# Kernel optimization log

Hardware: AMD Instinct MI355X
Metric: run time of the kernel (lower is better)

Reference implementation:

```python
import jax, jax.numpy as jnp
import numpy as np

H = 1024      # hidden_size
NH = 16       # num_attention_heads
DK = H // NH  # head dim
C = 1024      # cyclic_size


def setup_inputs() -> dict:
    key = jax.random.key(0)
    ks = jax.random.split(key, 13)
    B, S = 2, 2048
    s = 1.0 / np.sqrt(H)
    inp = {
        "q": jax.random.normal(ks[0], (B, S, H), jnp.float32),
        "k": jax.random.normal(ks[1], (B, S, H), jnp.float32),
        "v": jax.random.normal(ks[2], (B, S, H), jnp.float32),
        "Wq": jax.random.normal(ks[3], (H, H), jnp.float32) * s,
        "bq": jnp.zeros((H,), jnp.float32),
        "Wk": jax.random.normal(ks[4], (H, H), jnp.float32) * s,
        "bk": jnp.zeros((H,), jnp.float32),
        "Wv": jax.random.normal(ks[5], (H, H), jnp.float32) * s,
        "bv": jnp.zeros((H,), jnp.float32),
        "Wo": jax.random.normal(ks[6], (H, H), jnp.float32) * s,
        "bo": jnp.zeros((H,), jnp.float32),
        "Wc": jax.random.normal(ks[7], (H, C), jnp.float32) * s,
        "bc": jnp.zeros((C,), jnp.float32),
    }
    return inp


def _split_heads(x):
    B, S, _ = x.shape
    return x.reshape(B, S, NH, DK).transpose(0, 2, 1, 3)  # [B,NH,S,DK]


def reference(q, k, v, Wq, bq, Wk, bk, Wv, bv, Wo, bo, Wc, bc):
    Q = _split_heads(q @ Wq + bq)
    K = _split_heads(k @ Wk + bk)
    V = _split_heads(v @ Wv + bv)
    # unfused SDPA: full [B,NH,S,S] scores, as in the original module
    scores = jnp.einsum("bhqd,bhkd->bhqk", Q, K) / jnp.sqrt(jnp.float32(DK))
    probs = jax.nn.softmax(scores, axis=-1)
    attn = jnp.einsum("bhqk,bhkd->bhqd", probs, V)  # [B,NH,S,DK]
    B, _, S, _ = attn.shape
    merged = attn.transpose(0, 2, 1, 3).reshape(B, S, H)
    h = merged @ Wo + bo
    c = merged @ Wc + bc
    return (c, h)
```

## Files before the change

kernel.cpp:

```cpp
#include <hip/hip_runtime.h>
#include <stdint.h>

typedef unsigned short u16;
typedef short bf16x8 __attribute__((ext_vector_type(8)));
typedef short bf16x4 __attribute__((ext_vector_type(4)));
typedef float f32x4 __attribute__((ext_vector_type(4)));

#define MB (1u<<20)
#define CL2 0.18033688f

static __device__ __forceinline__ u16 f2bf(float x){
  union { float f; unsigned u; } v; v.f = x;
  return (u16)((v.u + 0x7FFFu + ((v.u >> 16) & 1u)) >> 16);
}

static __device__ __forceinline__ void gld_lds16(const void* g, void* l){
  __builtin_amdgcn_global_load_lds((const __attribute__((address_space(1))) unsigned int*)g,
                                   (__attribute__((address_space(3))) unsigned int*)l, 16, 0, 0);
}

__global__ void convx(const float* __restrict__ q, const float* __restrict__ k, const float* __restrict__ v,
                      u16* __restrict__ qb, u16* __restrict__ kb, u16* __restrict__ vb){
  const float* s = blockIdx.z==0 ? q : (blockIdx.z==1 ? k : v);
  u16* d = blockIdx.z==0 ? qb : (blockIdx.z==1 ? kb : vb);
  int i = (blockIdx.x*256 + threadIdx.x)*4;
  float4 f = *(const float4*)(s + i);
  ushort4 o; o.x=f2bf(f.x); o.y=f2bf(f.y); o.z=f2bf(f.z); o.w=f2bf(f.w);
  *(ushort4*)(d + i) = o;
}

__global__ void convw(const float* W0,const float* W1,const float* W2,const float* W3,const float* W4,
                      u16* T0,u16* T1,u16* T2,u16* T3,u16* T4){
  const float* W = blockIdx.z==0?W0:blockIdx.z==1?W1:blockIdx.z==2?W2:blockIdx.z==3?W3:W4;
  u16* T = blockIdx.z==0?T0:blockIdx.z==1?T1:blockIdx.z==2?T2:blockIdx.z==3?T3:T4;
  __shared__ u16 t[64][65];
  int k0 = blockIdx.x*64, n0 = blockIdx.y*64;
  for (int i=0;i<16;i++){
    int idx = i*256 + threadIdx.x;
    int r = idx >> 6, c = idx & 63;
    t[r][c] = f2bf(W[(size_t)(k0+r)*1024 + n0 + c]);
  }
  __syncthreads();
  for (int i=0;i<2;i++){
    int idx = i*256 + threadIdx.x;
    int nl = idx >> 3, kc = idx & 7;
    bf16x8 o;
    #pragma unroll
    for (int j=0;j<8;j++) o[j] = (short)t[kc*8+j][nl];
    *(bf16x8*)(T + (size_t)(n0+nl)*1024 + k0 + kc*8) = o;
  }
}

template<int MODE>
static __device__ __forceinline__ void gemm_bt_dev(const u16* __restrict__ A, const u16* __restrict__ Bt,
                                                   const float* __restrict__ bias, void* __restrict__ Cout){
  __shared__ u16 As[128*32];
  __shared__ u16 Bs[128*32];
  const int tid = threadIdx.x, lane = tid & 63, w = tid >> 6;
  const int wm = w >> 1, wn = w & 1, quad = lane >> 4, lr = lane & 15;
  const int m0 = blockIdx.y * 128, n0 = blockIdx.x * 128;
  f32x4 acc[4][4] = {};
  const u16* Ab = A + (size_t)m0*1024;
  const u16* Bb = Bt + (size_t)n0*1024;
  const int srow = w*16 + (lane>>2);
  const int sg   = (lane & 3);
  for (int k0 = 0; k0 < 1024; k0 += 32){
    #pragma unroll
    for (int r = 0; r < 2; ++r){
      int row = r*64 + srow;
      int g = sg ^ ((row>>1)&3);
      gld_lds16(Ab + (size_t)row*1024 + k0 + g*8, As + (r*64 + w*16)*32);
      gld_lds16(Bb + (size_t)row*1024 + k0 + g*8, Bs + (r*64 + w*16)*32);
    }
    __syncthreads();
    bf16x8 af[4], bfr[4];
    #pragma unroll
    for (int i=0;i<4;i++){
      int rowa = wm*64 + i*16 + lr;
      af[i] = *(const bf16x8*)(As + rowa*32 + ((quad ^ ((rowa>>1)&3))*8));
      int rowb = wn*64 + i*16 + lr;
      bfr[i] = *(const bf16x8*)(Bs + rowb*32 + ((quad ^ ((rowb>>1)&3))*8));
    }
    #pragma unroll
    for (int mi=0;mi<4;mi++)
      #pragma unroll
      for (int ni=0;ni<4;ni++)
        acc[mi][ni] = __builtin_amdgcn_mfma_f32_16x16x32_bf16(af[mi], bfr[ni], acc[mi][ni], 0, 0, 0);
    __syncthreads();
  }
  #pragma unroll
  for (int mi=0;mi<4;mi++){
    int row = m0 + wm*64 + mi*16 + quad*4;
    #pragma unroll
    for (int ni=0;ni<4;ni++){
      int col = n0 + wn*64 + ni*16 + lr;
      float bb = bias[col];
      #pragma unroll
      for (int rg=0; rg<4; rg++){
        float vv = acc[mi][ni][rg] + bb;
        int r = row + rg;
        if (MODE == 0){
          ((u16*)Cout)[(size_t)r*1024 + col] = f2bf(vv);
        } else if (MODE == 4){
          ((u16*)Cout)[(size_t)r*1024 + col] = f2bf(vv * CL2);
        } else if (MODE == 1){
          ((float*)Cout)[(size_t)r*1024 + col] = vv;
        } else if (MODE == 2){
          int b2 = r >> 11, s = r & 2047, kb2 = s >> 7, kvl = s & 127;
          int hh = col >> 6, hg = (col & 63) >> 3, hl = col & 7;
          ((u16*)Cout)[((size_t)(b2*16+hh)*16 + kb2)*8192 + hg*1024 + kvl*8 + hl] = f2bf(vv);
        } else {
          int b2 = r >> 11, s = r & 2047, kb2 = s >> 7, kvl = s & 127;
          int sgv = kvl >> 2, sl = kvl & 3;
          int hh = col >> 6, dd = col & 63;
          ((u16*)Cout)[((size_t)(b2*16+hh)*16 + kb2)*8192 + sgv*256 + dd*4 + sl] = f2bf(vv);
        }
      }
    }
  }
}

__global__ void qkv_gemm(const u16* qb,const u16* kb,const u16* vb,
                         const u16* Wqt,const u16* Wkt,const u16* Wvt,
                         const float* bq,const float* bk,const float* bv,
                         u16* Qb,u16* Kr,u16* Vr){
  if (blockIdx.z == 0)      gemm_bt_dev<4>(qb, Wqt, bq, Qb);
  else if (blockIdx.z == 1) gemm_bt_dev<2>(kb, Wkt, bk, Kr);
  else                      gemm_bt_dev<3>(vb, Wvt, bv, Vr);
}

__global__ void out_gemm(const u16* Mg, const u16* Wct, const u16* Wot,
                         const float* bc, const float* bo, float* out){
  const u16* B = blockIdx.z==0? Wct : Wot;
  const float* bias = blockIdx.z==0? bc : bo;
  float* C = out + (blockIdx.z==0? 0 : 4194304);
  gemm_bt_dev<1>(Mg, B, bias, C);
}

__global__ __launch_bounds__(256,2) void attn(const u16* __restrict__ Qb, const u16* __restrict__ Kr,
                                              const u16* __restrict__ Vr, u16* __restrict__ Mg){
  __shared__ u16 Ks[2][8192];
  __shared__ u16 Vs[2][8192];
  const int qt = blockIdx.x, bh = blockIdx.y, b = bh >> 4, h = bh & 15;
  const int tid = threadIdx.x, lane = tid & 63, w = tid >> 6;
  const int quad = lane >> 4, lr = lane & 15;
  const int q0 = qt*128 + w*32;

  bf16x8 aq[2][2];
  #pragma unroll
  for (int t=0;t<2;t++)
    #pragma unroll
    for (int ks=0;ks<2;ks++)
      aq[t][ks] = *(const bf16x8*)(Qb + (size_t)(b*2048 + q0 + t*16 + lr)*1024 + h*64 + ks*32 + quad*8);

  f32x4 acco[2][4] = {};
  f32x4 accl[2] = {};
  const bf16x4 ones = {(short)0x3F80,(short)0x3F80,(short)0x3F80,(short)0x3F80};

  const u16* Krb = Kr + (size_t)bh*131072;
  const u16* Vrb = Vr + (size_t)bh*131072;

  #pragma unroll
  for (int j=0;j<4;j++){
    gld_lds16(Krb + j*2048 + tid*8, &Ks[0][j*2048 + w*512]);
    gld_lds16(Vrb + j*2048 + tid*8, &Vs[0][j*2048 + w*512]);
  }

  for (int kb = 0; kb < 16; kb++){
    __syncthreads();
    const int cur = kb & 1;
    if (kb < 15){
      const u16* kg = Krb + (size_t)(kb+1)*8192;
      const u16* vg = Vrb + (size_t)(kb+1)*8192;
      #pragma unroll
      for (int j=0;j<4;j++){
        gld_lds16(kg + j*2048 + tid*8, &Ks[cur^1][j*2048 + w*512]);
        gld_lds16(vg + j*2048 + tid*8, &Vs[cur^1][j*2048 + w*512]);
      }
    }
    const u16* Ksc = Ks[cur];
    const u16* Vsc = Vs[cur];

    f32x4 accs[2][8] = {};
    #pragma unroll
    for (int ks=0;ks<2;ks++){
      #pragma unroll
      for (int mt=0;mt<8;mt++){
        bf16x8 kf = *(const bf16x8*)(Ksc + (ks*4+quad)*1024 + (mt*16+lr)*8);
        accs[0][mt] = __builtin_amdgcn_mfma_f32_16x16x32_bf16(kf, aq[0][ks], accs[0][mt], 0,0,0);
        accs[1][mt] = __builtin_amdgcn_mfma_f32_16x16x32_bf16(kf, aq[1][ks], accs[1][mt], 0,0,0);
      }
    }

    bf16x4 pf[2][8];
    #pragma unroll
    for (int t=0;t<2;t++){
      #pragma unroll
      for (int mt=0;mt<8;mt++){
        float p0 = __builtin_amdgcn_exp2f(accs[t][mt][0]);
        float p1 = __builtin_amdgcn_exp2f(accs[t][mt][1]);
        float p2 = __builtin_amdgcn_exp2f(accs[t][mt][2]);
        float p3 = __builtin_amdgcn_exp2f(accs[t][mt][3]);
        unsigned u0 = __float_as_uint(p0) + 0x8000u;
        unsigned u1 = __float_as_uint(p1) + 0x8000u;
        unsigned u2 = __float_as_uint(p2) + 0x8000u;
        unsigned u3 = __float_as_uint(p3) + 0x8000u;
        union { int2 i2; bf16x4 v; } pk;
        pk.i2.x = (int)__builtin_amdgcn_perm(u1, u0, 0x07060302u);
        pk.i2.y = (int)__builtin_amdgcn_perm(u3, u2, 0x07060302u);
        pf[t][mt] = pk.v;
      }
    }

    #pragma unroll
    for (int mt=0;mt<8;mt++){
      accl[0] = __builtin_amdgcn_mfma_f32_16x16x16bf16_1k(ones, pf[0][mt], accl[0], 0,0,0);
      accl[1] = __builtin_amdgcn_mfma_f32_16x16x16bf16_1k(ones, pf[1][mt], accl[1], 0,0,0);
    }

    #pragma unroll
    for (int dt=0;dt<4;dt++){
      #pragma unroll
      for (int mt=0;mt<8;mt++){
        bf16x4 vf = *(const bf16x4*)(Vsc + (mt*4+quad)*256 + (dt*16+lr)*4);
        acco[0][dt] = __builtin_amdgcn_mfma_f32_16x16x16bf16_1k(vf, pf[0][mt], acco[0][dt], 0,0,0);
        acco[1][dt] = __builtin_amdgcn_mfma_f32_16x16x16bf16_1k(vf, pf[1][mt], acco[1][dt], 0,0,0);
      }
    }
  }

  #pragma unroll
  for (int t=0;t<2;t++){
    float inv = 1.f / accl[t][0];
    u16* dst = Mg + (size_t)(b*2048 + q0 + t*16 + lr)*1024 + h*64;
    #pragma unroll
    for (int dt=0;dt<4;dt++){
      bf16x4 o;
      #pragma unroll
      for (int rg=0;rg<4;rg++) o[rg] = (short)f2bf(acco[t][dt][rg]*inv);
      *(bf16x4*)(dst + dt*16 + quad*4) = o;
    }
  }
}

extern "C" void kernel_launch(void* const* d_in, const int* in_sizes, int n_in,
                              void* d_out, int out_size, void* d_ws, size_t ws_size,
                              hipStream_t stream){
  const float* q  = (const float*)d_in[0];
  const float* k  = (const float*)d_in[1];
  const float* v  = (const float*)d_in[2];
  const float* Wq = (const float*)d_in[3];
  const float* bq = (const float*)d_in[4];
  const float* Wk = (const float*)d_in[5];
  const float* bk = (const float*)d_in[6];
  const float* Wv = (const float*)d_in[7];
  const float* bv = (const float*)d_in[8];
  const float* Wo = (const float*)d_in[9];
  const float* bo = (const float*)d_in[10];
  const float* Wc = (const float*)d_in[11];
  const float* bc = (const float*)d_in[12];
  char* ws = (char*)d_ws;
  u16* qb  = (u16*)(ws + (size_t)0*MB);
  u16* kb  = (u16*)(ws + (size_t)8*MB);
  u16* vb  = (u16*)(ws + (size_t)16*MB);
  u16* Wqt = (u16*)(ws + (size_t)24*MB);
  u16* Wkt = (u16*)(ws + (size_t)26*MB);
  u16* Wvt = (u16*)(ws + (size_t)28*MB);
  u16* Wot = (u16*)(ws + (size_t)30*MB);
  u16* Wct = (u16*)(ws + (size_t)32*MB);
  u16* Qb  = (u16*)(ws + (size_t)34*MB);
  u16* Kr  = (u16*)(ws + (size_t)42*MB);
  u16* Vr  = (u16*)(ws + (size_t)50*MB);
  u16* Mg  = (u16*)(ws + (size_t)58*MB);

  dim3 blk(256,1,1);
  hipLaunchKernelGGL(convx,    dim3(4096,1,3), blk, 0, stream, q,k,v, qb,kb,vb);
  hipLaunchKernelGGL(convw,    dim3(16,16,5),  blk, 0, stream, Wq,Wk,Wv,Wo,Wc, Wqt,Wkt,Wvt,Wot,Wct);
  hipLaunchKernelGGL(qkv_gemm, dim3(8,32,3),   blk, 0, stream, qb,kb,vb, Wqt,Wkt,Wvt, bq,bk,bv, Qb,Kr,Vr);
  hipLaunchKernelGGL(attn,     dim3(16,32,1),  blk, 0, stream, Qb, Kr, Vr, Mg);
  hipLaunchKernelGGL(out_gemm, dim3(8,32,2),   blk, 0, stream, Mg, Wct, Wot, bc, bo, (float*)d_out);
}
```

Before: 243.2 us.

## Split attention over two KV halves and combine partial results

Attention now splits the key/value sequence into two halves processed by separate blocks (grid z=2), using 64-row KV tiles and a smaller LDS footprint so four blocks can share a CU. Each half writes unnormalized bf16 outputs and row sums, and a new combine kernel adds them and normalizes. This doubles the block count to improve occupancy and latency hiding. The cost is an extra kernel launch, extra global traffic for the partial outputs, and an additional bf16 rounding of the unnormalized partial outputs. The softmax still has no max subtraction, so both halves share a scale and can be summed directly.

```diff
diff --git a/kernel.cpp b/kernel.cpp
--- a/kernel.cpp
+++ b/kernel.cpp
@@ -12,6 +12,9 @@
 static __device__ __forceinline__ u16 f2bf(float x){
   union { float f; unsigned u; } v; v.f = x;
   return (u16)((v.u + 0x7FFFu + ((v.u >> 16) & 1u)) >> 16);
+}
+static __device__ __forceinline__ float bf2f(u16 x){
+  union { unsigned u; float f; } v; v.u = ((unsigned)x) << 16; return v.f;
 }
 
 static __device__ __forceinline__ void gld_lds16(const void* g, void* l){
@@ -106,14 +109,14 @@
         } else if (MODE == 1){
           ((float*)Cout)[(size_t)r*1024 + col] = vv;
         } else if (MODE == 2){
-          int b2 = r >> 11, s = r & 2047, kb2 = s >> 7, kvl = s & 127;
+          int b2 = r >> 11, s = r & 2047, kb2 = s >> 6, kvl = s & 63;
           int hh = col >> 6, hg = (col & 63) >> 3, hl = col & 7;
-          ((u16*)Cout)[((size_t)(b2*16+hh)*16 + kb2)*8192 + hg*1024 + kvl*8 + hl] = f2bf(vv);
+          ((u16*)Cout)[((size_t)(b2*16+hh)*32 + kb2)*4096 + hg*512 + kvl*8 + hl] = f2bf(vv);
         } else {
-          int b2 = r >> 11, s = r & 2047, kb2 = s >> 7, kvl = s & 127;
+          int b2 = r >> 11, s = r & 2047, kb2 = s >> 6, kvl = s & 63;
           int sgv = kvl >> 2, sl = kvl & 3;
           int hh = col >> 6, dd = col & 63;
-          ((u16*)Cout)[((size_t)(b2*16+hh)*16 + kb2)*8192 + sgv*256 + dd*4 + sl] = f2bf(vv);
+          ((u16*)Cout)[((size_t)(b2*16+hh)*32 + kb2)*4096 + sgv*256 + dd*4 + sl] = f2bf(vv);
         }
       }
     }
@@ -137,11 +140,14 @@
   gemm_bt_dev<1>(Mg, B, bias, C);
 }
 
-__global__ __launch_bounds__(256,2) void attn(const u16* __restrict__ Qb, const u16* __restrict__ Kr,
-                                              const u16* __restrict__ Vr, u16* __restrict__ Mg){
-  __shared__ u16 Ks[2][8192];
-  __shared__ u16 Vs[2][8192];
-  const int qt = blockIdx.x, bh = blockIdx.y, b = bh >> 4, h = bh & 15;
+__global__ __launch_bounds__(256,4) void attn(const u16* __restrict__ Qb, const u16* __restrict__ Kr,
+                                              const u16* __restrict__ Vr,
+                                              u16* __restrict__ O0, u16* __restrict__ O1,
+                                              float* __restrict__ l0, float* __restrict__ l1){
+  __shared__ u16 Ks[2][4096];
+  __shared__ u16 Vs[2][4096];
+  const int qt = blockIdx.x, bh = blockIdx.y, sp = blockIdx.z;
+  const int b = bh >> 4, h = bh & 15;
   const int tid = threadIdx.x, lane = tid & 63, w = tid >> 6;
   const int quad = lane >> 4, lr = lane & 15;
   const int q0 = qt*128 + w*32;
@@ -157,11 +163,11 @@
   f32x4 accl[2] = {};
   const bf16x4 ones = {(short)0x3F80,(short)0x3F80,(short)0x3F80,(short)0x3F80};
 
-  const u16* Krb = Kr + (size_t)bh*131072;
-  const u16* Vrb = Vr + (size_t)bh*131072;
-
-  #pragma unroll
-  for (int j=0;j<4;j++){
+  const u16* Krb = Kr + (size_t)bh*131072 + (size_t)sp*65536;
+  const u16* Vrb = Vr + (size_t)bh*131072 + (size_t)sp*65536;
+
+  #pragma unroll
+  for (int j=0;j<2;j++){
     gld_lds16(Krb + j*2048 + tid*8, &Ks[0][j*2048 + w*512]);
     gld_lds16(Vrb + j*2048 + tid*8, &Vs[0][j*2048 + w*512]);
   }
@@ -170,10 +176,10 @@
     __syncthreads();
     const int cur = kb & 1;
     if (kb < 15){
-      const u16* kg = Krb + (size_t)(kb+1)*8192;
-      const u16* vg = Vrb + (size_t)(kb+1)*8192;
-      #pragma unroll
-      for (int j=0;j<4;j++){
+      const u16* kg = Krb + (size_t)(kb+1)*4096;
+      const u16* vg = Vrb + (size_t)(kb+1)*4096;
+      #pragma unroll
+      for (int j=0;j<2;j++){
         gld_lds16(kg + j*2048 + tid*8, &Ks[cur^1][j*2048 + w*512]);
         gld_lds16(vg + j*2048 + tid*8, &Vs[cur^1][j*2048 + w*512]);
       }
@@ -181,26 +187,23 @@
     const u16* Ksc = Ks[cur];
     const u16* Vsc = Vs[cur];
 
-    f32x4 accs[2][8] = {};
-    #pragma unroll
-    for (int ks=0;ks<2;ks++){
-      #pragma unroll
-      for (int mt=0;mt<8;mt++){
-        bf16x8 kf = *(const bf16x8*)(Ksc + (ks*4+quad)*1024 + (mt*16+lr)*8);
-        accs[0][mt] = __builtin_amdgcn_mfma_f32_16x16x32_bf16(kf, aq[0][ks], accs[0][mt], 0,0,0);
-        accs[1][mt] = __builtin_amdgcn_mfma_f32_16x16x32_bf16(kf, aq[1][ks], accs[1][mt], 0,0,0);
-      }
-    }
-
-    bf16x4 pf[2][8];
-    #pragma unroll
-    for (int t=0;t<2;t++){
-      #pragma unroll
-      for (int mt=0;mt<8;mt++){
-        float p0 = __builtin_amdgcn_exp2f(accs[t][mt][0]);
-        float p1 = __builtin_amdgcn_exp2f(accs[t][mt][1]);
-        float p2 = __builtin_amdgcn_exp2f(accs[t][mt][2]);
-        float p3 = __builtin_amdgcn_exp2f(accs[t][mt][3]);
+    bf16x4 pf[2][4];
+    #pragma unroll
+    for (int mt=0;mt<4;mt++){
+      bf16x8 kf0 = *(const bf16x8*)(Ksc + quad*512     + (mt*16+lr)*8);
+      bf16x8 kf1 = *(const bf16x8*)(Ksc + (4+quad)*512 + (mt*16+lr)*8);
+      f32x4 a0 = {}, a1 = {};
+      a0 = __builtin_amdgcn_mfma_f32_16x16x32_bf16(kf0, aq[0][0], a0, 0,0,0);
+      a1 = __builtin_amdgcn_mfma_f32_16x16x32_bf16(kf0, aq[1][0], a1, 0,0,0);
+      a0 = __builtin_amdgcn_mfma_f32_16x16x32_bf16(kf1, aq[0][1], a0, 0,0,0);
+      a1 = __builtin_amdgcn_mfma_f32_16x16x32_bf16(kf1, aq[1][1], a1, 0,0,0);
+      #pragma unroll
+      for (int t=0;t<2;t++){
+        const f32x4& a = t ? a1 : a0;
+        float p0 = __builtin_amdgcn_exp2f(a[0]);
+        float p1 = __builtin_amdgcn_exp2f(a[1]);
+        float p2 = __builtin_amdgcn_exp2f(a[2]);
+        float p3 = __builtin_amdgcn_exp2f(a[3]);
         unsigned u0 = __float_as_uint(p0) + 0x8000u;
         unsigned u1 = __float_as_uint(p1) + 0x8000u;
         unsigned u2 = __float_as_uint(p2) + 0x8000u;
@@ -213,7 +216,7 @@
     }
 
     #pragma unroll
-    for (int mt=0;mt<8;mt++){
+    for (int mt=0;mt<4;mt++){
       accl[0] = __builtin_amdgcn_mfma_f32_16x16x16bf16_1k(ones, pf[0][mt], accl[0], 0,0,0);
       accl[1] = __builtin_amdgcn_mfma_f32_16x16x16bf16_1k(ones, pf[1][mt], accl[1], 0,0,0);
     }
@@ -221,7 +224,7 @@
     #pragma unroll
     for (int dt=0;dt<4;dt++){
       #pragma unroll
-      for (int mt=0;mt<8;mt++){
+      for (int mt=0;mt<4;mt++){
         bf16x4 vf = *(const bf16x4*)(Vsc + (mt*4+quad)*256 + (dt*16+lr)*4);
         acco[0][dt] = __builtin_amdgcn_mfma_f32_16x16x16bf16_1k(vf, pf[0][mt], acco[0][dt], 0,0,0);
         acco[1][dt] = __builtin_amdgcn_mfma_f32_16x16x16bf16_1k(vf, pf[1][mt], acco[1][dt], 0,0,0);
@@ -229,18 +232,37 @@
     }
   }
 
+  u16* Op = sp ? O1 : O0;
+  float* lp = sp ? l1 : l0;
   #pragma unroll
   for (int t=0;t<2;t++){
-    float inv = 1.f / accl[t][0];
-    u16* dst = Mg + (size_t)(b*2048 + q0 + t*16 + lr)*1024 + h*64;
+    u16* dst = Op + (size_t)(b*2048 + q0 + t*16 + lr)*1024 + h*64;
     #pragma unroll
     for (int dt=0;dt<4;dt++){
       bf16x4 o;
       #pragma unroll
-      for (int rg=0;rg<4;rg++) o[rg] = (short)f2bf(acco[t][dt][rg]*inv);
+      for (int rg=0;rg<4;rg++) o[rg] = (short)f2bf(acco[t][dt][rg]);
       *(bf16x4*)(dst + dt*16 + quad*4) = o;
     }
-  }
+    if (quad == 0) lp[(size_t)bh*2048 + q0 + t*16 + lr] = accl[t][0];
+  }
+}
+
+__global__ void combine(const u16* __restrict__ O0, const u16* __restrict__ O1,
+                        const float* __restrict__ l0, const float* __restrict__ l1,
+                        u16* __restrict__ Mg){
+  int i = (blockIdx.x*256 + threadIdx.x)*8;
+  int row = i >> 10, col = i & 1023;
+  int b = row >> 11, q = row & 2047, h = col >> 6;
+  size_t li = (size_t)(b*16+h)*2048 + q;
+  float inv = 1.f / (l0[li] + l1[li]);
+  bf16x8 a = *(const bf16x8*)(O0 + i);
+  bf16x8 c = *(const bf16x8*)(O1 + i);
+  bf16x8 o;
+  #pragma unroll
+  for (int j=0;j<8;j++)
+    o[j] = (short)f2bf((bf2f((u16)a[j]) + bf2f((u16)c[j])) * inv);
+  *(bf16x8*)(Mg + i) = o;
 }
 
 extern "C" void kernel_launch(void* const* d_in, const int* in_sizes, int n_in,
@@ -272,11 +294,16 @@
   u16* Kr  = (u16*)(ws + (size_t)42*MB);
   u16* Vr  = (u16*)(ws + (size_t)50*MB);
   u16* Mg  = (u16*)(ws + (size_t)58*MB);
+  u16* O0  = (u16*)(ws + (size_t)0*MB);
+  u16* O1  = (u16*)(ws + (size_t)8*MB);
+  float* l0 = (float*)(ws + (size_t)16*MB);
+  float* l1 = (float*)(ws + (size_t)17*MB);
 
   dim3 blk(256,1,1);
   hipLaunchKernelGGL(convx,    dim3(4096,1,3), blk, 0, stream, q,k,v, qb,kb,vb);
   hipLaunchKernelGGL(convw,    dim3(16,16,5),  blk, 0, stream, Wq,Wk,Wv,Wo,Wc, Wqt,Wkt,Wvt,Wot,Wct);
   hipLaunchKernelGGL(qkv_gemm, dim3(8,32,3),   blk, 0, stream, qb,kb,vb, Wqt,Wkt,Wvt, bq,bk,bv, Qb,Kr,Vr);
-  hipLaunchKernelGGL(attn,     dim3(16,32,1),  blk, 0, stream, Qb, Kr, Vr, Mg);
+  hipLaunchKernelGGL(attn,     dim3(16,32,2),  blk, 0, stream, Qb, Kr, Vr, O0, O1, l0, l1);
+  hipLaunchKernelGGL(combine,  dim3(2048,1,1), blk, 0, stream, O0, O1, l0, l1, Mg);
   hipLaunchKernelGGL(out_gemm, dim3(8,32,2),   blk, 0, stream, Mg, Wct, Wot, bc, bo, (float*)d_out);
 }
```

Result: slower. 248.4 us (+2.1%).
